# Optimization experiments

Measured on AMD Instinct MI355X. Metric: run time of the kernel, lower is better.

Reference implementation:

```python
import jax, jax.numpy as jnp
import numpy as np

LMAX = 8                         # lmax-1 used by s2/so3 irreps
DIMS = [2 * l + 1 for l in range(LMAX + 1)]
S2_OFF = np.cumsum([0] + DIMS).tolist()            # offsets into 81-dim s2 irreps
SO3_OFF = np.cumsum([0] + [d * d for d in DIMS]).tolist()  # offsets into 969-dim so3 irreps
S2_DIM = S2_OFF[-1]              # 81
SO3_DIM = SO3_OFF[-1]            # 969
F_IN = 81                        # multiplicity into S2Conv
F_SO3 = 300
C = 768                          # encoder feature channels
KS = 7                           # encoder feature map / kernel size
B = 8
G_S2 = 48                        # s2 healpix grid rec_level=1
G_ACT = 4096                     # SO3Activation grid points (stand-in for res=20 grid)
G_SO3 = 36864                    # so3 healpix grid rec_level=3


def setup_inputs() -> dict:
    key = jax.random.key(0)
    ks = jax.random.split(key, 7)
    return {
        "x": jax.random.normal(ks[0], (B, C, KS, KS), jnp.float32),
        "F": jax.random.normal(ks[1], (F_IN, S2_DIM * C, KS, KS), jnp.float32) * 0.02,
        "w_s2": jax.random.normal(ks[2], (F_IN, F_SO3, G_S2), jnp.float32) * 0.1,
        "Y": jax.random.normal(ks[3], (G_S2, S2_DIM), jnp.float32),
        "w_so3": jax.random.normal(ks[4], (F_SO3, 1, G_SO3), jnp.float32) * 0.1,
        "D": jax.random.normal(ks[5], (G_SO3, SO3_DIM), jnp.float32),
        "D_act": jax.random.normal(ks[6], (G_ACT, SO3_DIM), jnp.float32),
    }


def _forward(x, F, w_s2, Y, w_so3, D, D_act):
    b = x.shape[0]
    # ---- Induction layer: split expanded R2Conv filter into 768-channel chunks,
    # stack, contract with feature map. g_split: (n=81, c_out=81, C, 7, 7)
    g = jnp.swapaxes(F.reshape(F_IN, S2_DIM, C, KS, KS), 0, 1)
    y = jnp.einsum('ijkhw,akhw->aji', g, x)          # (B, 81, 81): (batch, f_in, s2 irreps)

    # ---- S2Conv: expand kernel into irrep space, per-l block linear (s2 -> so3 irreps)
    psi = jnp.einsum('ni,xyn->xyi', Y, w_s2) / np.sqrt(G_S2)  # (81, 300, 81)
    outs = []
    for l, d in enumerate(DIMS):
        o = S2_OFF[l]
        xl = y[:, :, o:o + d]                        # (B, f_in, 2l+1)
        wl = psi[:, :, o:o + d]                      # (f_in, f_out, mul_out=2l+1)
        ol = jnp.einsum('bfm,fgu->bgum', xl, wl) / np.sqrt(F_IN)
        outs.append(ol.reshape(b, F_SO3, d * d))
    z = jnp.concatenate(outs, axis=-1)               # (B, 300, 969)

    # ---- SO3Activation: to grid, relu, back to irreps
    s = jnp.einsum('bfi,gi->bfg', z, D_act)
    z = jnp.einsum('bfg,gi->bfi', jax.nn.relu(s), D_act) / G_ACT

    # ---- SO3Conv: expand kernel via Wigner-D buffer, per-l block linear (so3 -> so3)
    psi2 = jnp.einsum('ni,xyn->xyi', D, w_so3) / np.sqrt(G_SO3)  # (300, 1, 969)
    outs = []
    for l, d in enumerate(DIMS):
        o = SO3_OFF[l]
        xl = z[:, :, o:o + d * d].reshape(b, F_SO3, d, d)   # (B, f, u, m)
        wl = psi2[:, :, o:o + d * d].reshape(F_SO3, 1, d, d)  # (f, g, v, u)
        ol = jnp.einsum('bfum,fgvu->bgvm', xl, wl) / np.sqrt(F_SO3 * d)
        outs.append(ol.reshape(b, 1, d * d))
    return jnp.concatenate(outs, axis=-1)            # (B, 1, 969)


def reference(x, F, w_s2, Y, w_so3, D, D_act):
    return _forward(x, F, w_s2, Y, w_so3, D, D_act)
```

## Files before the change

kernel.cpp:

```cpp
#include <hip/hip_runtime.h>
#include <hip/hip_bf16.h>
#include <math.h>

#define THREADS 256

constexpr int B_    = 8;
constexpr int C_    = 768;
constexpr int KS_   = 7;
constexpr int F_IN  = 81;
constexpr int F_SO3 = 300;
constexpr int S2_DIM  = 81;
constexpr int SO3_DIM = 969;
constexpr int G_S2  = 48;
constexpr int G_ACT = 4096;
constexpr int G_SO3 = 36864;
constexpr int CKK   = C_ * KS_ * KS_;
constexpr int CKK4  = CKK / 4;
constexpr int NPAIR = F_IN * S2_DIM;

constexpr int D2_SPLIT = 4;
constexpr int E1_SPLIT = 16;
constexpr int F_SPLIT  = 5;

__constant__ int d_S2_OFF[10]  = {0, 1, 4, 9, 16, 25, 36, 49, 64, 81};
__constant__ int d_SO3_OFF[10] = {0, 1, 10, 35, 84, 165, 286, 455, 680, 969};

struct CEnt { unsigned char u, m, so, l; };
struct CLut { CEnt v[992]; };
constexpr CLut make_clut() {
  CLut t{};
  int S2O[10]  = {0, 1, 4, 9, 16, 25, 36, 49, 64, 81};
  int SO3O[10] = {0, 1, 10, 35, 84, 165, 286, 455, 680, 969};
  for (int i = 0; i < 969; ++i) {
    int l = 0;
    while (i >= SO3O[l + 1]) ++l;
    int d = 2 * l + 1, r = i - SO3O[l];
    t.v[i].u  = (unsigned char)(r / d);
    t.v[i].m  = (unsigned char)(r % d);
    t.v[i].so = (unsigned char)S2O[l];
    t.v[i].l  = (unsigned char)l;
  }
  return t;
}
__constant__ CLut g_clut = make_clut();

using short8 = __attribute__((ext_vector_type(8))) short;
using f32x4  = __attribute__((ext_vector_type(4))) float;
using f4v    = __attribute__((ext_vector_type(4))) float;

#define GL16(gp, lp)                                                        \
  __builtin_amdgcn_global_load_lds(                                         \
      (const __attribute__((address_space(1))) void*)(gp),                  \
      (__attribute__((address_space(3))) void*)(lp), 16, 0, 0)

constexpr size_t AL(size_t x) { return (x + 1023) & ~(size_t)1023; }
constexpr size_t O_Y     = 0;
constexpr size_t O_PSI   = O_Y     + AL((size_t)8 * NPAIR * 4);
constexpr size_t O_ZBF   = O_PSI   + AL((size_t)F_IN * F_SO3 * 81 * 4);
constexpr size_t O_DACT  = O_ZBF   + AL((size_t)2432 * 1024 * 2);
constexpr size_t O_DACTT = O_DACT  + AL((size_t)4096 * 1024 * 2);
constexpr size_t O_WSO3  = O_DACTT + AL((size_t)1024 * 4096 * 2);
constexpr size_t O_DT    = O_WSO3  + AL((size_t)384 * 36864 * 2);
constexpr size_t O_SBF   = O_DT    + AL((size_t)1024 * 36864 * 2);
constexpr size_t O_D2P   = O_SBF   + AL((size_t)2432 * 4096 * 2);
constexpr size_t O_E1P   = O_D2P   + AL((size_t)D2_SPLIT * 2432 * 1024 * 4);
constexpr size_t O_PSI2  = O_E1P   + AL((size_t)E1_SPLIT * 384 * 1024 * 4);
constexpr size_t O_SFP   = O_PSI2  + AL((size_t)F_SO3 * SO3_DIM * 4);
constexpr size_t FAST_NEED = O_SFP + AL((size_t)F_SPLIT * 8 * SO3_DIM * 4);

constexpr size_t WS_Y    = 0;
constexpr size_t WS_PSI  = 52488;
constexpr size_t WS_Z    = 2020788;
constexpr size_t WS_S    = 4346388;
constexpr size_t WS_Z2   = 14176788;
constexpr size_t WS_P2P  = 16502388;
constexpr size_t WS_PSI2 = 18827988;

__global__ __launch_bounds__(THREADS) void k_stage_a3(
    const float* __restrict__ Fm, const float* __restrict__ x, float* __restrict__ y) {
  const int p0  = blockIdx.x * 3;
  const int tid = threadIdx.x;
  const f4v* __restrict__ F4 = (const f4v*)Fm;
  const f4v* __restrict__ x4 = (const f4v*)x;

  float acc[3][8];
#pragma unroll
  for (int p = 0; p < 3; ++p)
#pragma unroll
    for (int b = 0; b < 8; ++b) acc[p][b] = 0.f;

  for (int i = tid; i < CKK4; i += THREADS) {
    f4v xv[8];
#pragma unroll
    for (int b = 0; b < 8; ++b) xv[b] = x4[b * CKK4 + i];
#pragma unroll
    for (int p = 0; p < 3; ++p) {
      f4v fv = __builtin_nontemporal_load(&F4[(size_t)(p0 + p) * CKK4 + i]);
#pragma unroll
      for (int b = 0; b < 8; ++b)
        acc[p][b] += fv[0] * xv[b][0] + fv[1] * xv[b][1] + fv[2] * xv[b][2] + fv[3] * xv[b][3];
    }
  }

  __shared__ float red[4][24];
  const int lane = tid & 63, wid = tid >> 6;
#pragma unroll
  for (int p = 0; p < 3; ++p) {
#pragma unroll
    for (int b = 0; b < 8; ++b) {
      float v = acc[p][b];
      v += __shfl_down(v, 32);
      v += __shfl_down(v, 16);
      v += __shfl_down(v, 8);
      v += __shfl_down(v, 4);
      v += __shfl_down(v, 2);
      v += __shfl_down(v, 1);
      if (lane == 0) red[wid][p * 8 + b] = v;
    }
  }
  __syncthreads();
  if (tid < 24) {
    float v = red[0][tid] + red[1][tid] + red[2][tid] + red[3][tid];
    int p = tid / 8, b = tid % 8;
    y[(size_t)b * NPAIR + p0 + p] = v;
  }
}

__device__ __forceinline__ void cvt_body(const float* __restrict__ src,
                                         __hip_bfloat16* __restrict__ dst,
                                         int R, int Cs, int Cp, int blk) {
  size_t idx = (size_t)blk * THREADS + threadIdx.x;
  int r = (int)(idx / (unsigned)Cp), c = (int)(idx % (unsigned)Cp);
  float v = (r < R && c < Cs) ? src[(size_t)r * Cs + c] : 0.f;
  dst[idx] = __float2bfloat16(v);
}

__device__ __forceinline__ void tr_body(const float* __restrict__ src,
                                        __hip_bfloat16* __restrict__ dst,
                                        int R, int Cs, size_t dstStride, int bx, int by) {
  __shared__ float tile[32][33];
  const int c0 = bx * 32, r0 = by * 32;
  const int tx = threadIdx.x & 31, ty = threadIdx.x >> 5;
#pragma unroll
  for (int i = 0; i < 32; i += 8) {
    int r = r0 + ty + i, c = c0 + tx;
    tile[ty + i][tx] = (r < R && c < Cs) ? src[(size_t)r * Cs + c] : 0.f;
  }
  __syncthreads();
#pragma unroll
  for (int i = 0; i < 32; i += 8) {
    int c = c0 + ty + i, r = r0 + tx;
    if (c < Cs && r < R) dst[(size_t)c * dstStride + r] = __float2bfloat16(tile[tx][ty + i]);
  }
}

__device__ __forceinline__ void psi_body(const float* __restrict__ w_s2,
                                         const float* __restrict__ Y,
                                         float* __restrict__ psi, int blk) {
  int idx = blk * THREADS + threadIdx.x;
  if (idx >= F_IN * F_SO3 * S2_DIM) return;
  int s  = idx % S2_DIM;
  int fg = idx / S2_DIM;
  const float* w = w_s2 + (size_t)fg * G_S2;
  float acc = 0.f;
#pragma unroll 8
  for (int n = 0; n < G_S2; ++n) acc += w[n] * Y[n * S2_DIM + s];
  psi[idx] = acc * 0.14433756729740643f;
}

constexpr int UB1 = 16384;
constexpr int UB2 = 3968;
constexpr int UB3 = 55296;
constexpr int UB4 = 35712;
constexpr int UB5 = 7689;
constexpr int UB_TOT = UB1 + UB2 + UB3 + UB4 + UB5;

__global__ __launch_bounds__(THREADS) void k_uber(
    const float* __restrict__ D_act, __hip_bfloat16* __restrict__ Dact_bf,
    __hip_bfloat16* __restrict__ DactT_bf,
    const float* __restrict__ w_so3, __hip_bfloat16* __restrict__ wso3_bf,
    const float* __restrict__ D, __hip_bfloat16* __restrict__ DT_bf,
    const float* __restrict__ w_s2, const float* __restrict__ Y, float* __restrict__ psi) {
  int b = blockIdx.x;
  if (b < UB1) { cvt_body(D_act, Dact_bf, G_ACT, SO3_DIM, 1024, b); return; }
  b -= UB1;
  if (b < UB2) { tr_body(D_act, DactT_bf, G_ACT, SO3_DIM, 4096, b % 31, b / 31); return; }
  b -= UB2;
  if (b < UB3) { cvt_body(w_so3, wso3_bf, F_SO3, G_SO3, G_SO3, b); return; }
  b -= UB3;
  if (b < UB4) { tr_body(D, DT_bf, G_SO3, SO3_DIM, 36864, b % 31, b / 31); return; }
  b -= UB4;
  psi_body(w_s2, Y, psi, b);
}

__global__ __launch_bounds__(THREADS) void k_stage_c_bf(
    const float* __restrict__ y, const float* __restrict__ psi, __hip_bfloat16* __restrict__ z) {
  const int b = blockIdx.x / F_SO3;
  const int g = blockIdx.x % F_SO3;
  __shared__ float ybl[NPAIR];
  __shared__ float psl[NPAIR];
  const int tid = threadIdx.x;
  for (int t = tid; t < NPAIR; t += THREADS) {
    ybl[t] = y[(size_t)b * NPAIR + t];
    int f = t / S2_DIM, s = t % S2_DIM;
    psl[t] = psi[((size_t)f * F_SO3 + g) * S2_DIM + s];
  }
  __syncthreads();
  for (int i = tid; i < 1024; i += THREADS) {
    float acc = 0.f;
    if (i < SO3_DIM) {
      CEnt e = g_clut.v[i];
      int im = e.so + e.m, iu = e.so + e.u;
#pragma unroll 9
      for (int f = 0; f < F_IN; ++f)
        acc += ybl[f * S2_DIM + im] * psl[f * S2_DIM + iu];
      acc *= (1.0f / 9.0f);
    }
    z[((size_t)b * F_SO3 + g) * 1024 + i] = __float2bfloat16(acc);
  }
}

struct GemmDesc {
  const __hip_bfloat16* A;
  const __hip_bfloat16* B;
  void* C;
  int K, kSpan, Ncols;
  float scale;
  size_t splitStride;
  int gx, gy, gz, epi;
};

__device__ __forceinline__ void mfma_nt_body(const GemmDesc g, unsigned lin) {
  __shared__ __align__(16) char smem[32768];
  char* As = smem;
  char* Bs = smem + 16384;

  unsigned nwg = (unsigned)(g.gx * g.gy * g.gz);
  if ((nwg & 7u) == 0u) {
    unsigned q = nwg >> 3;
    lin = (lin & 7u) * q + (lin >> 3);
  }
  const int bxi = (int)(lin % (unsigned)g.gx);
  const unsigned t1 = lin / (unsigned)g.gx;
  const int byi = (int)(t1 % (unsigned)g.gy);
  const int bzi = (int)(t1 / (unsigned)g.gy);

  const int t    = threadIdx.x;
  const int lane = t & 63;
  const int wave = t >> 6;
  const int wr   = wave >> 1, wc = wave & 1;
  const int bm = byi * 128, bn = bxi * 128;
  const int kBegin = bzi * g.kSpan;
  const int kEnd   = kBegin + g.kSpan;

  const char* pA[4];
  const char* pB[4];
  int ldsOff[4];
#pragma unroll
  for (int i = 0; i < 4; ++i) {
    int L   = i * 4096 + t * 16;
    int row = L >> 7;
    int kb  = (L & 127) ^ ((row & 7) << 4);
    pA[i] = (const char*)g.A + ((size_t)(bm + row) * g.K) * 2 + kb;
    pB[i] = (const char*)g.B + ((size_t)(bn + row) * g.K) * 2 + kb;
    ldsOff[i] = L;
  }

  f32x4 acc[4][4] = {};

  for (int k0 = kBegin; k0 < kEnd; k0 += 64) {
    size_t koff = (size_t)k0 * 2;
#pragma unroll
    for (int i = 0; i < 4; ++i) {
      GL16(pA[i] + koff, As + ldsOff[i]);
      GL16(pB[i] + koff, Bs + ldsOff[i]);
    }
    __syncthreads();
#pragma unroll
    for (int kk = 0; kk < 2; ++kk) {
      const int klin = kk * 64 + ((lane >> 4) << 4);
      short8 af[4], bfr[4];
#pragma unroll
      for (int m = 0; m < 4; ++m) {
        int ra = (wr << 6) + (m << 4) + (lane & 15);
        af[m] = *(const short8*)(As + ra * 128 + (klin ^ ((ra & 7) << 4)));
        int rb = (wc << 6) + (m << 4) + (lane & 15);
        bfr[m] = *(const short8*)(Bs + rb * 128 + (klin ^ ((rb & 7) << 4)));
      }
#pragma unroll
      for (int m = 0; m < 4; ++m)
#pragma unroll
        for (int n = 0; n < 4; ++n)
          acc[m][n] = __builtin_amdgcn_mfma_f32_16x16x32_bf16(af[m], bfr[n], acc[m][n], 0, 0, 0);
    }
    __syncthreads();
  }

  const int rbase = bm + (wr << 6) + ((lane >> 4) << 2);
  const int cbase = bn + (wc << 6) + (lane & 15);
  if (g.epi == 0) {
    float* C = (float*)g.C + (size_t)bzi * g.splitStride;
#pragma unroll
    for (int m = 0; m < 4; ++m)
#pragma unroll
      for (int n = 0; n < 4; ++n)
#pragma unroll
        for (int r = 0; r < 4; ++r)
          C[(size_t)(rbase + m * 16 + r) * g.Ncols + (cbase + n * 16)] = acc[m][n][r] * g.scale;
  } else {
    __hip_bfloat16* C = (__hip_bfloat16*)g.C;
#pragma unroll
    for (int m = 0; m < 4; ++m)
#pragma unroll
      for (int n = 0; n < 4; ++n)
#pragma unroll
        for (int r = 0; r < 4; ++r)
          C[(size_t)(rbase + m * 16 + r) * g.Ncols + (cbase + n * 16)] =
              __float2bfloat16(fmaxf(acc[m][n][r], 0.f));
  }
}

__global__ __launch_bounds__(THREADS) void k_mfma_dual(GemmDesc g0, GemmDesc g1, int n0) {
  if ((int)blockIdx.x < n0) mfma_nt_body(g0, blockIdx.x);
  else                      mfma_nt_body(g1, blockIdx.x - n0);
}

__global__ __launch_bounds__(THREADS) void k_mfma_reduce(
    GemmDesc g, int n0,
    const float* __restrict__ parts, float* __restrict__ dst, int R, int C,
    size_t rowStride, size_t splitStride, size_t dstStride, int nSplit, float scale) {
  if ((int)blockIdx.x < n0) { mfma_nt_body(g, blockIdx.x); return; }
  int idx = (int)(blockIdx.x - n0) * THREADS + threadIdx.x;
  if (idx >= R * C) return;
  int r = idx / C, c = idx % C;
  float a = 0.f;
  for (int s = 0; s < nSplit; ++s) a += parts[(size_t)s * splitStride + (size_t)r * rowStride + c];
  dst[(size_t)r * dstStride + c] = a * scale;
}

__global__ __launch_bounds__(THREADS) void k_stage_f_part(
    const float* __restrict__ d2p, const float* __restrict__ psi2, float* __restrict__ partial) {
  const int b  = blockIdx.x / 9;
  const int l  = blockIdx.x % 9;
  const int sp = blockIdx.y;
  const int d = 2 * l + 1, d2 = d * d;
  const int off = d_SO3_OFF[l];
  constexpr size_t SS = (size_t)2432 * 1024;
  __shared__ float zb[10][289];
  __shared__ float pb[10][289];
  const int tid = threadIdx.x;
  float acc[2] = {0.f, 0.f};
  const int fBeg = sp * (F_SO3 / F_SPLIT), fEnd = fBeg + F_SO3 / F_SPLIT;
  for (int fc = fBeg; fc < fEnd; fc += 10) {
    for (int t = tid; t < 10 * d2; t += THREADS) {
      int fl = t / d2, q = t - fl * d2;
      int f  = fc + fl;
      size_t zi = ((size_t)b * F_SO3 + f) * 1024 + off + q;
      float zv = d2p[zi] + d2p[zi + SS] + d2p[zi + 2 * SS] + d2p[zi + 3 * SS];
      zb[fl][q] = zv * (1.0f / G_ACT);
      pb[fl][q] = psi2[(size_t)f * SO3_DIM + off + q];
    }
    __syncthreads();
#pragma unroll 2
    for (int io = 0; io < 2; ++io) {
      int i = tid + io * THREADS;
      if (i < d2) {
        int v = i / d, m = i - v * d;
        float a = acc[io];
#pragma unroll
        for (int fl = 0; fl < 10; ++fl) {
          float s_ = 0.f;
          for (int u = 0; u < d; ++u)
            s_ += zb[fl][u * d + m] * pb[fl][v * d + u];
          a += s_;
        }
        acc[io] = a;
      }
    }
    __syncthreads();
  }
  for (int io = 0; io < 2; ++io) {
    int i = tid + io * THREADS;
    if (i < d2) partial[((size_t)sp * 8 + b) * SO3_DIM + off + i] = acc[io];
  }
}

__global__ __launch_bounds__(THREADS) void k_stage_f_red(
    const float* __restrict__ partial, float* __restrict__ out) {
  int idx = blockIdx.x * THREADS + threadIdx.x;
  if (idx >= 8 * SO3_DIM) return;
  int b = idx / SO3_DIM, i = idx % SO3_DIM;
  int l = g_clut.v[i].l;
  float a = 0.f;
#pragma unroll
  for (int sp = 0; sp < F_SPLIT; ++sp)
    a += partial[((size_t)sp * 8 + b) * SO3_DIM + i];
  out[(size_t)b * SO3_DIM + i] = a * rsqrtf(300.0f * (float)(2 * l + 1));
}

__global__ __launch_bounds__(THREADS) void k_psi(
    const float* __restrict__ w_s2, const float* __restrict__ Y, float* __restrict__ psi) {
  psi_body(w_s2, Y, psi, blockIdx.x);
}

__global__ __launch_bounds__(THREADS) void k_stage_c(
    const float* __restrict__ y, const float* __restrict__ psi, float* __restrict__ z) {
  const int b = blockIdx.x / F_SO3;
  const int g = blockIdx.x % F_SO3;
  __shared__ float ybl[NPAIR];
  __shared__ float psl[NPAIR];
  const int tid = threadIdx.x;
  for (int t = tid; t < NPAIR; t += THREADS) {
    ybl[t] = y[(size_t)b * NPAIR + t];
    int f = t / S2_DIM, s = t % S2_DIM;
    psl[t] = psi[((size_t)f * F_SO3 + g) * S2_DIM + s];
  }
  __syncthreads();
  for (int i = tid; i < SO3_DIM; i += THREADS) {
    CEnt e = g_clut.v[i];
    int im = e.so + e.m, iu = e.so + e.u;
    float acc = 0.f;
#pragma unroll 9
    for (int f = 0; f < F_IN; ++f)
      acc += ybl[f * S2_DIM + im] * psl[f * S2_DIM + iu];
    z[((size_t)b * F_SO3 + g) * SO3_DIM + i] = acc * (1.0f / 9.0f);
  }
}

__global__ __launch_bounds__(THREADS) void k_gemm_nt_relu(
    const float* __restrict__ A, const float* __restrict__ Bm, float* __restrict__ Cm,
    int M, int N, int K) {
  __shared__ float As[16][68];
  __shared__ float Bs[16][68];
  const int bm = blockIdx.y * 64, bn = blockIdx.x * 64;
  const int t  = threadIdx.x;
  const int lk = t & 15, lm = t >> 4;
  const int tn = t & 15, tm = t >> 4;
  float acc[4][4] = {};
  for (int k0 = 0; k0 < K; k0 += 16) {
    int gk = k0 + lk;
#pragma unroll
    for (int j = 0; j < 4; ++j) {
      int m  = lm + 16 * j;
      int gm = bm + m;
      As[lk][m] = (gm < M && gk < K) ? A[(size_t)gm * K + gk] : 0.f;
      int gn = bn + m;
      Bs[lk][m] = (gn < N && gk < K) ? Bm[(size_t)gn * K + gk] : 0.f;
    }
    __syncthreads();
#pragma unroll
    for (int k = 0; k < 16; ++k) {
      float4 av = *(const float4*)&As[k][tm * 4];
      float4 bv = *(const float4*)&Bs[k][tn * 4];
      float a[4] = {av.x, av.y, av.z, av.w};
      float bb[4] = {bv.x, bv.y, bv.z, bv.w};
#pragma unroll
      for (int i2 = 0; i2 < 4; ++i2)
#pragma unroll
        for (int j2 = 0; j2 < 4; ++j2)
          acc[i2][j2] += a[i2] * bb[j2];
    }
    __syncthreads();
  }
#pragma unroll
  for (int i2 = 0; i2 < 4; ++i2) {
    int gm = bm + tm * 4 + i2;
    if (gm >= M) continue;
#pragma unroll
    for (int j2 = 0; j2 < 4; ++j2) {
      int gn = bn + tn * 4 + j2;
      if (gn < N) Cm[(size_t)gm * N + gn] = fmaxf(acc[i2][j2], 0.f);
    }
  }
}

__global__ __launch_bounds__(THREADS) void k_gemm_nn(
    const float* __restrict__ A, const float* __restrict__ Bm, float* __restrict__ Cm,
    int M, int N, int K, int kSpan, float scale, size_t cStride) {
  __shared__ float As[16][68];
  __shared__ float Bs[16][68];
  const int bm = blockIdx.y * 64, bn = blockIdx.x * 64;
  const int t   = threadIdx.x;
  const int lk  = t & 15, lm = t >> 4;
  const int ln  = t & 63, lkq = t >> 6;
  const int tn  = t & 15, tm = t >> 4;
  const int kBegin = blockIdx.z * kSpan;
  const int kEnd   = kBegin + kSpan;
  float* C = Cm + (size_t)blockIdx.z * cStride;
  float acc[4][4] = {};
  for (int k0 = kBegin; k0 < kEnd; k0 += 16) {
    {
      int gk = k0 + lk;
#pragma unroll
      for (int j = 0; j < 4; ++j) {
        int m = lm + 16 * j, gm = bm + m;
        As[lk][m] = (gm < M) ? A[(size_t)gm * K + gk] : 0.f;
      }
    }
    {
      int gn = bn + ln;
#pragma unroll
      for (int j = 0; j < 4; ++j) {
        int k = lkq + 4 * j;
        Bs[k][ln] = (gn < N) ? Bm[(size_t)(k0 + k) * N + gn] : 0.f;
      }
    }
    __syncthreads();
#pragma unroll
    for (int k = 0; k < 16; ++k) {
      float4 av = *(const float4*)&As[k][tm * 4];
      float4 bv = *(const float4*)&Bs[k][tn * 4];
      float a[4] = {av.x, av.y, av.z, av.w};
      float bb[4] = {bv.x, bv.y, bv.z, bv.w};
#pragma unroll
      for (int i2 = 0; i2 < 4; ++i2)
#pragma unroll
        for (int j2 = 0; j2 < 4; ++j2)
          acc[i2][j2] += a[i2] * bb[j2];
    }
    __syncthreads();
  }
#pragma unroll
  for (int i2 = 0; i2 < 4; ++i2) {
    int gm = bm + tm * 4 + i2;
    if (gm >= M) continue;
#pragma unroll
    for (int j2 = 0; j2 < 4; ++j2) {
      int gn = bn + tn * 4 + j2;
      if (gn < N) C[(size_t)gm * N + gn] = acc[i2][j2] * scale;
    }
  }
}

__global__ __launch_bounds__(THREADS) void k_reduce_psi2(
    const float* __restrict__ parts, float* __restrict__ psi2) {
  int idx = blockIdx.x * THREADS + threadIdx.x;
  if (idx >= F_SO3 * SO3_DIM) return;
  float acc = 0.f;
#pragma unroll
  for (int s = 0; s < 8; ++s) acc += parts[(size_t)s * (F_SO3 * SO3_DIM) + idx];
  psi2[idx] = acc * (1.0f / 192.0f);
}

__global__ __launch_bounds__(THREADS) void k_stage_f(
    const float* __restrict__ z2, const float* __restrict__ psi2, float* __restrict__ out,
    int zStride) {
  const int b = blockIdx.x / 9;
  const int l = blockIdx.x % 9;
  const int d = 2 * l + 1, d2 = d * d;
  const int off = d_SO3_OFF[l];
  __shared__ float zb[10][289];
  __shared__ float pb[10][289];
  const int tid = threadIdx.x;
  float acc[2] = {0.f, 0.f};
  const float scale = rsqrtf(300.0f * (float)d);
  for (int fc = 0; fc < F_SO3; fc += 10) {
    for (int t = tid; t < 10 * d2; t += THREADS) {
      int fl = t / d2, q = t - fl * d2;
      int f  = fc + fl;
      zb[fl][q] = z2[((size_t)b * F_SO3 + f) * zStride + off + q];
      pb[fl][q] = psi2[(size_t)f * SO3_DIM + off + q];
    }
    __syncthreads();
#pragma unroll 2
    for (int io = 0; io < 2; ++io) {
      int i = tid + io * THREADS;
      if (i < d2) {
        int v = i / d, m = i - v * d;
        float a = acc[io];
#pragma unroll
        for (int fl = 0; fl < 10; ++fl) {
          float s_ = 0.f;
          for (int u = 0; u < d; ++u)
            s_ += zb[fl][u * d + m] * pb[fl][v * d + u];
          a += s_;
        }
        acc[io] = a;
      }
    }
    __syncthreads();
  }
  for (int io = 0; io < 2; ++io) {
    int i = tid + io * THREADS;
    if (i < d2) out[(size_t)b * SO3_DIM + off + i] = acc[io] * scale;
  }
}

extern "C" void kernel_launch(void* const* d_in, const int* in_sizes, int n_in,
                              void* d_out, int out_size, void* d_ws, size_t ws_size,
                              hipStream_t stream) {
  const float* x     = (const float*)d_in[0];
  const float* Fm    = (const float*)d_in[1];
  const float* w_s2  = (const float*)d_in[2];
  const float* Y     = (const float*)d_in[3];
  const float* w_so3 = (const float*)d_in[4];
  const float* D     = (const float*)d_in[5];
  const float* D_act = (const float*)d_in[6];
  float* out = (float*)d_out;

  if (ws_size >= FAST_NEED) {
    char* p = (char*)d_ws;
    float*          y       = (float*)(p + O_Y);
    float*          psi     = (float*)(p + O_PSI);
    __hip_bfloat16* z_bf    = (__hip_bfloat16*)(p + O_ZBF);
    __hip_bfloat16* Dact_bf = (__hip_bfloat16*)(p + O_DACT);
    __hip_bfloat16* DactT_bf= (__hip_bfloat16*)(p + O_DACTT);
    __hip_bfloat16* wso3_bf = (__hip_bfloat16*)(p + O_WSO3);
    __hip_bfloat16* DT_bf   = (__hip_bfloat16*)(p + O_DT);
    __hip_bfloat16* s_bf    = (__hip_bfloat16*)(p + O_SBF);
    float*          d2p     = (float*)(p + O_D2P);
    float*          e1p     = (float*)(p + O_E1P);
    float*          psi2    = (float*)(p + O_PSI2);
    float*          sfp     = (float*)(p + O_SFP);

    k_stage_a3<<<NPAIR / 3, THREADS, 0, stream>>>(Fm, x, y);
    k_uber<<<UB_TOT, THREADS, 0, stream>>>(
        D_act, Dact_bf, DactT_bf, w_so3, wso3_bf, D, DT_bf, w_s2, Y, psi);
    k_stage_c_bf<<<B_ * F_SO3, THREADS, 0, stream>>>(y, psi, z_bf);

    GemmDesc e1{wso3_bf, DT_bf, e1p, G_SO3, G_SO3 / E1_SPLIT, 1024, 1.f,
                (size_t)384 * 1024, 8, 3, E1_SPLIT, 0};
    GemmDesc d1{z_bf, Dact_bf, s_bf, 1024, 1024, 4096, 1.f, 0, 32, 19, 1, 1};
    int nE1 = 8 * 3 * E1_SPLIT;
    int nD1 = 32 * 19;
    k_mfma_dual<<<nE1 + nD1, THREADS, 0, stream>>>(e1, d1, nE1);

    GemmDesc d2{s_bf, DactT_bf, d2p, 4096, 4096 / D2_SPLIT, 1024, 1.f,
                (size_t)2432 * 1024, 8, 19, D2_SPLIT, 0};
    int nD2 = 8 * 19 * D2_SPLIT;
    int nE1r = (F_SO3 * SO3_DIM + THREADS - 1) / THREADS;
    k_mfma_reduce<<<nD2 + nE1r, THREADS, 0, stream>>>(
        d2, nD2, e1p, psi2, F_SO3, SO3_DIM, 1024, (size_t)384 * 1024, SO3_DIM,
        E1_SPLIT, 1.0f / 192.0f);

    k_stage_f_part<<<dim3(B_ * 9, F_SPLIT), THREADS, 0, stream>>>(d2p, psi2, sfp);
    k_stage_f_red<<<(8 * SO3_DIM + THREADS - 1) / THREADS, THREADS, 0, stream>>>(sfp, out);
  } else {
    float* ws  = (float*)d_ws;
    float* y    = ws + WS_Y;
    float* psi  = ws + WS_PSI;
    float* z    = ws + WS_Z;
    float* s    = ws + WS_S;
    float* z2   = ws + WS_Z2;
    float* p2p  = ws + WS_P2P;
    float* psi2 = ws + WS_PSI2;

    k_stage_a3<<<NPAIR / 3, THREADS, 0, stream>>>(Fm, x, y);
    k_psi<<<(F_IN * F_SO3 * S2_DIM + THREADS - 1) / THREADS, THREADS, 0, stream>>>(w_s2, Y, psi);
    k_stage_c<<<B_ * F_SO3, THREADS, 0, stream>>>(y, psi, z);
    k_gemm_nt_relu<<<dim3(G_ACT / 64, (B_ * F_SO3 + 63) / 64), THREADS, 0, stream>>>(
        z, D_act, s, B_ * F_SO3, G_ACT, SO3_DIM);
    k_gemm_nn<<<dim3((SO3_DIM + 63) / 64, (B_ * F_SO3 + 63) / 64, 1), THREADS, 0, stream>>>(
        s, D_act, z2, B_ * F_SO3, SO3_DIM, G_ACT, G_ACT, 1.0f / G_ACT, 0);
    k_gemm_nn<<<dim3((SO3_DIM + 63) / 64, (F_SO3 + 63) / 64, 8), THREADS, 0, stream>>>(
        w_so3, D, p2p, F_SO3, SO3_DIM, G_SO3, G_SO3 / 8, 1.0f, (size_t)F_SO3 * SO3_DIM);
    k_reduce_psi2<<<(F_SO3 * SO3_DIM + THREADS - 1) / THREADS, THREADS, 0, stream>>>(p2p, psi2);
    k_stage_f<<<B_ * 9, THREADS, 0, stream>>>(z2, psi2, out, SO3_DIM);
  }
}
```

Measured before the change: 611.0 us.

## Vectorize conversions, unroll stage A loads, transpose psi layout, share LDS

Result: no change. 613.8 us (+0.5%).

```diff
diff --git a/kernel.cpp b/kernel.cpp
--- a/kernel.cpp
+++ b/kernel.cpp
@@ -76,7 +76,7 @@
 constexpr size_t WS_P2P  = 16502388;
 constexpr size_t WS_PSI2 = 18827988;
 
-__global__ __launch_bounds__(THREADS) void k_stage_a3(
+__global__ __launch_bounds__(THREADS, 4) void k_stage_a3(
     const float* __restrict__ Fm, const float* __restrict__ x, float* __restrict__ y) {
   const int p0  = blockIdx.x * 3;
   const int tid = threadIdx.x;
@@ -89,16 +89,35 @@
 #pragma unroll
     for (int b = 0; b < 8; ++b) acc[p][b] = 0.f;
 
-  for (int i = tid; i < CKK4; i += THREADS) {
-    f4v xv[8];
-#pragma unroll
-    for (int b = 0; b < 8; ++b) xv[b] = x4[b * CKK4 + i];
+  int i = tid;
+  for (int it = 0; it < 18; ++it, i += 2 * THREADS) {
+    f4v xv0[8], xv1[8];
+#pragma unroll
+    for (int b = 0; b < 8; ++b) {
+      xv0[b] = x4[b * CKK4 + i];
+      xv1[b] = x4[b * CKK4 + i + THREADS];
+    }
 #pragma unroll
     for (int p = 0; p < 3; ++p) {
-      f4v fv = __builtin_nontemporal_load(&F4[(size_t)(p0 + p) * CKK4 + i]);
+      f4v fv0 = __builtin_nontemporal_load(&F4[(size_t)(p0 + p) * CKK4 + i]);
+      f4v fv1 = __builtin_nontemporal_load(&F4[(size_t)(p0 + p) * CKK4 + i + THREADS]);
+#pragma unroll
+      for (int b = 0; b < 8; ++b) {
+        acc[p][b] += fv0[0] * xv0[b][0] + fv0[1] * xv0[b][1] + fv0[2] * xv0[b][2] + fv0[3] * xv0[b][3];
+        acc[p][b] += fv1[0] * xv1[b][0] + fv1[1] * xv1[b][1] + fv1[2] * xv1[b][2] + fv1[3] * xv1[b][3];
+      }
+    }
+  }
+  if (i < CKK4) {
+    f4v xv0[8];
+#pragma unroll
+    for (int b = 0; b < 8; ++b) xv0[b] = x4[b * CKK4 + i];
+#pragma unroll
+    for (int p = 0; p < 3; ++p) {
+      f4v fv0 = __builtin_nontemporal_load(&F4[(size_t)(p0 + p) * CKK4 + i]);
 #pragma unroll
       for (int b = 0; b < 8; ++b)
-        acc[p][b] += fv[0] * xv[b][0] + fv[1] * xv[b][1] + fv[2] * xv[b][2] + fv[3] * xv[b][3];
+        acc[p][b] += fv0[0] * xv0[b][0] + fv0[1] * xv0[b][1] + fv0[2] * xv0[b][2] + fv0[3] * xv0[b][3];
     }
   }
 
@@ -126,51 +145,67 @@
   }
 }
 
-__device__ __forceinline__ void cvt_body(const float* __restrict__ src,
-                                         __hip_bfloat16* __restrict__ dst,
-                                         int R, int Cs, int Cp, int blk) {
-  size_t idx = (size_t)blk * THREADS + threadIdx.x;
-  int r = (int)(idx / (unsigned)Cp), c = (int)(idx % (unsigned)Cp);
-  float v = (r < R && c < Cs) ? src[(size_t)r * Cs + c] : 0.f;
-  dst[idx] = __float2bfloat16(v);
+__device__ __forceinline__ void cvt4_body(const float* __restrict__ src,
+                                          __hip_bfloat16* __restrict__ dst,
+                                          int R, int Cs, int Cp, int blk) {
+  size_t e0 = ((size_t)blk * THREADS + threadIdx.x) * 4;
+  int r = (int)(e0 / (unsigned)Cp), c = (int)(e0 % (unsigned)Cp);
+  __hip_bfloat16 o[4];
+#pragma unroll
+  for (int j = 0; j < 4; ++j) {
+    float v = (r < R && c + j < Cs) ? src[(size_t)r * Cs + c + j] : 0.f;
+    o[j] = __float2bfloat16(v);
+  }
+  *(ushort4*)(&dst[e0]) = *(const ushort4*)o;
 }
 
 __device__ __forceinline__ void tr_body(const float* __restrict__ src,
                                         __hip_bfloat16* __restrict__ dst,
-                                        int R, int Cs, size_t dstStride, int bx, int by) {
-  __shared__ float tile[32][33];
+                                        int R, int Cs, size_t dstStride, int bx, int by,
+                                        char* smemc) {
+  float (*tile)[33] = (float(*)[33])smemc;
   const int c0 = bx * 32, r0 = by * 32;
   const int tx = threadIdx.x & 31, ty = threadIdx.x >> 5;
 #pragma unroll
   for (int i = 0; i < 32; i += 8) {
     int r = r0 + ty + i, c = c0 + tx;
-    tile[ty + i][tx] = (r < R && c < Cs) ? src[(size_t)r * Cs + c] : 0.f;
+    tile[ty + i][tx] = (c < Cs) ? src[(size_t)r * Cs + c] : 0.f;
   }
   __syncthreads();
-#pragma unroll
-  for (int i = 0; i < 32; i += 8) {
-    int c = c0 + ty + i, r = r0 + tx;
-    if (c < Cs && r < R) dst[(size_t)c * dstStride + r] = __float2bfloat16(tile[tx][ty + i]);
+  const int rp = threadIdx.x & 15;
+  const int cl = threadIdx.x >> 4;
+#pragma unroll
+  for (int j = 0; j < 2; ++j) {
+    int cc = cl + 16 * j;
+    int c  = c0 + cc;
+    if (c < Cs) {
+      __hip_bfloat16 o[2];
+      o[0] = __float2bfloat16(tile[2 * rp][cc]);
+      o[1] = __float2bfloat16(tile[2 * rp + 1][cc]);
+      *(ushort2*)(&dst[(size_t)c * dstStride + r0 + 2 * rp]) = *(const ushort2*)o;
+    }
   }
 }
 
 __device__ __forceinline__ void psi_body(const float* __restrict__ w_s2,
                                          const float* __restrict__ Y,
-                                         float* __restrict__ psi, int blk) {
+                                         float* __restrict__ psi_t, int blk) {
   int idx = blk * THREADS + threadIdx.x;
   if (idx >= F_IN * F_SO3 * S2_DIM) return;
   int s  = idx % S2_DIM;
-  int fg = idx / S2_DIM;
-  const float* w = w_s2 + (size_t)fg * G_S2;
+  int t1 = idx / S2_DIM;
+  int f  = t1 % F_IN;
+  int g  = t1 / F_IN;
+  const float* w = w_s2 + ((size_t)f * F_SO3 + g) * G_S2;
   float acc = 0.f;
 #pragma unroll 8
   for (int n = 0; n < G_S2; ++n) acc += w[n] * Y[n * S2_DIM + s];
-  psi[idx] = acc * 0.14433756729740643f;
-}
-
-constexpr int UB1 = 16384;
+  psi_t[idx] = acc * 0.14433756729740643f;
+}
+
+constexpr int UB1 = 4096;
 constexpr int UB2 = 3968;
-constexpr int UB3 = 55296;
+constexpr int UB3 = 13824;
 constexpr int UB4 = 35712;
 constexpr int UB5 = 7689;
 constexpr int UB_TOT = UB1 + UB2 + UB3 + UB4 + UB5;
@@ -180,30 +215,32 @@
     __hip_bfloat16* __restrict__ DactT_bf,
     const float* __restrict__ w_so3, __hip_bfloat16* __restrict__ wso3_bf,
     const float* __restrict__ D, __hip_bfloat16* __restrict__ DT_bf,
-    const float* __restrict__ w_s2, const float* __restrict__ Y, float* __restrict__ psi) {
+    const float* __restrict__ w_s2, const float* __restrict__ Y, float* __restrict__ psi_t) {
+  __shared__ __align__(16) char smem[4352];
   int b = blockIdx.x;
-  if (b < UB1) { cvt_body(D_act, Dact_bf, G_ACT, SO3_DIM, 1024, b); return; }
+  if (b < UB1) { cvt4_body(D_act, Dact_bf, G_ACT, SO3_DIM, 1024, b); return; }
   b -= UB1;
-  if (b < UB2) { tr_body(D_act, DactT_bf, G_ACT, SO3_DIM, 4096, b % 31, b / 31); return; }
+  if (b < UB2) { tr_body(D_act, DactT_bf, G_ACT, SO3_DIM, 4096, b % 31, b / 31, smem); return; }
   b -= UB2;
-  if (b < UB3) { cvt_body(w_so3, wso3_bf, F_SO3, G_SO3, G_SO3, b); return; }
+  if (b < UB3) { cvt4_body(w_so3, wso3_bf, F_SO3, G_SO3, G_SO3, b); return; }
   b -= UB3;
-  if (b < UB4) { tr_body(D, DT_bf, G_SO3, SO3_DIM, 36864, b % 31, b / 31); return; }
+  if (b < UB4) { tr_body(D, DT_bf, G_SO3, SO3_DIM, 36864, b % 31, b / 31, smem); return; }
   b -= UB4;
-  psi_body(w_s2, Y, psi, b);
+  psi_body(w_s2, Y, psi_t, b);
 }
 
 __global__ __launch_bounds__(THREADS) void k_stage_c_bf(
-    const float* __restrict__ y, const float* __restrict__ psi, __hip_bfloat16* __restrict__ z) {
+    const float* __restrict__ y, const float* __restrict__ psi_t,
+    __hip_bfloat16* __restrict__ z) {
   const int b = blockIdx.x / F_SO3;
   const int g = blockIdx.x % F_SO3;
   __shared__ float ybl[NPAIR];
   __shared__ float psl[NPAIR];
   const int tid = threadIdx.x;
+  const float* pg = psi_t + (size_t)g * NPAIR;
   for (int t = tid; t < NPAIR; t += THREADS) {
     ybl[t] = y[(size_t)b * NPAIR + t];
-    int f = t / S2_DIM, s = t % S2_DIM;
-    psl[t] = psi[((size_t)f * F_SO3 + g) * S2_DIM + s];
+    psl[t] = pg[t];
   }
   __syncthreads();
   for (int i = tid; i < 1024; i += THREADS) {
@@ -230,8 +267,7 @@
   int gx, gy, gz, epi;
 };
 
-__device__ __forceinline__ void mfma_nt_body(const GemmDesc g, unsigned lin) {
-  __shared__ __align__(16) char smem[32768];
+__device__ __forceinline__ void mfma_nt_body(const GemmDesc g, unsigned lin, char* smem) {
   char* As = smem;
   char* Bs = smem + 16384;
 
@@ -321,15 +357,17 @@
 }
 
 __global__ __launch_bounds__(THREADS) void k_mfma_dual(GemmDesc g0, GemmDesc g1, int n0) {
-  if ((int)blockIdx.x < n0) mfma_nt_body(g0, blockIdx.x);
-  else                      mfma_nt_body(g1, blockIdx.x - n0);
+  __shared__ __align__(16) char smem[32768];
+  if ((int)blockIdx.x < n0) mfma_nt_body(g0, blockIdx.x, smem);
+  else                      mfma_nt_body(g1, blockIdx.x - n0, smem);
 }
 
 __global__ __launch_bounds__(THREADS) void k_mfma_reduce(
     GemmDesc g, int n0,
     const float* __restrict__ parts, float* __restrict__ dst, int R, int C,
     size_t rowStride, size_t splitStride, size_t dstStride, int nSplit, float scale) {
-  if ((int)blockIdx.x < n0) { mfma_nt_body(g, blockIdx.x); return; }
+  __shared__ __align__(16) char smem[32768];
+  if ((int)blockIdx.x < n0) { mfma_nt_body(g, blockIdx.x, smem); return; }
   int idx = (int)(blockIdx.x - n0) * THREADS + threadIdx.x;
   if (idx >= R * C) return;
   int r = idx / C, c = idx % C;
@@ -399,21 +437,21 @@
 }
 
 __global__ __launch_bounds__(THREADS) void k_psi(
-    const float* __restrict__ w_s2, const float* __restrict__ Y, float* __restrict__ psi) {
-  psi_body(w_s2, Y, psi, blockIdx.x);
+    const float* __restrict__ w_s2, const float* __restrict__ Y, float* __restrict__ psi_t) {
+  psi_body(w_s2, Y, psi_t, blockIdx.x);
 }
 
 __global__ __launch_bounds__(THREADS) void k_stage_c(
-    const float* __restrict__ y, const float* __restrict__ psi, float* __restrict__ z) {
+    const float* __restrict__ y, const float* __restrict__ psi_t, float* __restrict__ z) {
   const int b = blockIdx.x / F_SO3;
   const int g = blockIdx.x % F_SO3;
   __shared__ float ybl[NPAIR];
   __shared__ float psl[NPAIR];
   const int tid = threadIdx.x;
+  const float* pg = psi_t + (size_t)g * NPAIR;
   for (int t = tid; t < NPAIR; t += THREADS) {
     ybl[t] = y[(size_t)b * NPAIR + t];
-    int f = t / S2_DIM, s = t % S2_DIM;
-    psl[t] = psi[((size_t)f * F_SO3 + g) * S2_DIM + s];
+    psl[t] = pg[t];
   }
   __syncthreads();
   for (int i = tid; i < SO3_DIM; i += THREADS) {
```
